# Kernel tuning notes

Measured on AMD Instinct MI355X. Metric: run time of the kernel, lower is better.

## Reference

```python
import jax, jax.numpy as jnp
import numpy as np

B, T, H = 16, 512, 384   # batch, phoneme length, hidden
F, K = 384, 3            # filter size, kernel size
DMAX = 8                 # max per-token duration
L = T * DMAX             # static max expanded length (original uses real_len.max())


def conv1d_same(x, w, b):
    # x: [B, T, Cin], w: [Cout, Cin, K] (torch OIW layout), padding = K//2 both sides
    y = jax.lax.conv_general_dilated(
        x.transpose(0, 2, 1), w, window_strides=(1,),
        padding=[(K // 2, K // 2)], dimension_numbers=('NCW', 'OIW', 'NCW'))
    return y.transpose(0, 2, 1) + b


def layer_norm(x, g, b, eps=1e-5):
    mu = jnp.mean(x, axis=-1, keepdims=True)
    var = jnp.mean(jnp.square(x - mu), axis=-1, keepdims=True)
    return (x - mu) * jax.lax.rsqrt(var + eps) * g + b


def setup_inputs() -> dict:
    key = jax.random.key(0)
    ks = jax.random.split(key, 10)
    x = jax.random.normal(ks[0], (B, T, H), dtype=jnp.float32)
    # log-durations whose exp().round() gives integers in [1, DMAX]
    dur = jax.random.randint(ks[1], (B, T), 1, DMAX + 1)
    true_durations = jnp.log(dur.astype(jnp.float32))
    s1 = 1.0 / np.sqrt(H * K)
    s2 = 1.0 / np.sqrt(F * K)
    s3 = 1.0 / np.sqrt(F)
    return {
        'x': x,
        'true_durations': true_durations,
        'conv1_w': jax.random.uniform(ks[2], (F, H, K), jnp.float32, -s1, s1),
        'conv1_b': jnp.zeros((F,), jnp.float32),
        'ln1_g': jnp.ones((F,), jnp.float32),
        'ln1_b': jnp.zeros((F,), jnp.float32),
        'conv2_w': jax.random.uniform(ks[3], (F, F, K), jnp.float32, -s2, s2),
        'conv2_b': jnp.zeros((F,), jnp.float32),
        'ln2_g': jnp.ones((F,), jnp.float32),
        'ln2_b': jnp.zeros((F,), jnp.float32),
        'lin_w': jax.random.uniform(ks[4], (F, 1), jnp.float32, -s3, s3),
        'lin_b': jnp.zeros((1,), jnp.float32),
    }


def reference(x, true_durations, conv1_w, conv1_b, ln1_g, ln1_b,
              conv2_w, conv2_b, ln2_g, ln2_b, lin_w, lin_b):
    # duration predictor net (dropout in eval mode = identity)
    h = conv1d_same(x, conv1_w, conv1_b)
    h = jax.nn.gelu(layer_norm(h, ln1_g, ln1_b), approximate=False)
    h = conv1d_same(h, conv2_w, conv2_b)
    h = jax.nn.gelu(layer_norm(h, ln2_g, ln2_b), approximate=False)
    length = jax.nn.relu(h @ lin_w + lin_b)[..., 0]  # [B, T]

    # length regulation with ground-truth durations (detached ints in original)
    dur = jnp.round(jnp.exp(true_durations)).astype(jnp.int32)  # [B, T]
    ends = jnp.cumsum(dur, axis=1)          # [B, T]
    starts = ends - dur                     # [B, T]
    k = jnp.arange(L)                       # [L]
    # binary alignment: A[b,t,l] = 1 iff starts[b,t] <= l < ends[b,t]
    A = ((k >= starts[..., None]) & (k < ends[..., None])).astype(x.dtype)  # [B,T,L]
    out = jnp.einsum('bth,btl->blh', x, A)  # = (x^T @ A)^T, [B, L, H]
    return out, length
```

## Files before the change

kernel.cpp:

```cpp
#include <hip/hip_runtime.h>
#include <stdint.h>

typedef unsigned short u16;
typedef unsigned int   u32;

#define B_    16
#define T_    512
#define H_    384
#define F_    384
#define DMAX_ 8
#define L_    4096
#define KD    1152
#define M_    8192

typedef __bf16 bf16x8 __attribute__((ext_vector_type(8)));
typedef float  f32x4  __attribute__((ext_vector_type(4)));

typedef __attribute__((address_space(1))) u32 gu32;
typedef __attribute__((address_space(3))) u32 lu32;

__device__ __forceinline__ void dma16(const void* g, void* l) {
    __builtin_amdgcn_global_load_lds((gu32*)(uintptr_t)g, (lu32*)(u32)(uintptr_t)l, 16, 0, 0);
}

__device__ __forceinline__ u16 f2b(float f) {
    union { float f; u32 i; } v; v.f = f;
    u32 x = v.i;
    return (u16)((x + 0x7fffu + ((x >> 16) & 1u)) >> 16);
}

__global__ void k_prep(const float* __restrict__ td, const float* __restrict__ w1,
                       const float* __restrict__ w2, const float* __restrict__ x,
                       int* __restrict__ tmap, u16* __restrict__ Wp1,
                       u16* __restrict__ Wp2, u16* __restrict__ xb,
                       u16* __restrict__ zp) {
    int blk = blockIdx.x, tid = threadIdx.x;
    if (blk < 16) {
        __shared__ int s[T_];
        int b = blk, t = tid;
        int d = (int)roundf(expf(td[b * T_ + t]));
        if (d < 0) d = 0; if (d > DMAX_) d = DMAX_;
        int v = d;
        s[t] = v;
        __syncthreads();
        for (int off = 1; off < T_; off <<= 1) {
            int add = (t >= off) ? s[t - off] : 0;
            __syncthreads();
            v += add;
            s[t] = v;
            __syncthreads();
        }
        int end = v, start = end - d;
        for (int i = start; i < end; ++i) tmap[b * L_ + i] = t;
        int total = s[T_ - 1];
        for (int l = total + t; l < L_; l += T_) tmap[b * L_ + l] = -1;
    } else if (blk == 16) {
        zp[tid] = 0;
    } else if (blk < 17 + 1728) {
        int j = (blk - 17) * 512 + tid;
        const int n = F_ * H_ * 3;
        const float* src = (j < n) ? w1 : w2;
        u16* dst         = (j < n) ? Wp1 : Wp2;
        int jj = (j < n) ? j : j - n;
        int f = jj / (H_ * 3);
        int rem = jj % (H_ * 3);
        int c = rem / 3, kk = rem % 3;
        dst[f * KD + kk * H_ + c] = f2b(src[jj]);
    } else {
        int v = (blk - 1745) * 512 + tid;
        float4 f = *(const float4*)(x + (size_t)v * 4);
        u16 o[4] = { f2b(f.x), f2b(f.y), f2b(f.z), f2b(f.w) };
        *(uint2*)(xb + (size_t)v * 4) = *(uint2*)o;
    }
}

__global__ void k_expand(const float* __restrict__ x, const int* __restrict__ tmap,
                         float* __restrict__ out) {
    int v = blockIdx.x * blockDim.x + threadIdx.x;
    if (v >= B_ * L_ * 96) return;
    int row = v / 96, c4 = v % 96;
    int b = row >> 12;
    int t = tmap[row];
    uint4 val = make_uint4(0u, 0u, 0u, 0u);
    if (t >= 0) val = *(const uint4*)(x + (size_t)((b << 9) + t) * H_ + c4 * 4);
    *(uint4*)(out + (size_t)row * H_ + c4 * 4) = val;
}

struct GemmCtx {
    const u16* abase[3];
    const u16* bbase[12];
    u16* destA;
    u16* destB[12];
    const u16* aptr[2][2];
    const u16* bptr[6][2];
};

__device__ __forceinline__ void gemm_core(u16* smem, const u16* __restrict__ src,
                                          const u16* __restrict__ Wp,
                                          const u16* __restrict__ zp,
                                          int m0, int tid, f32x4 acc[2][6]) {
    int w = tid >> 6, lane = tid & 63;
    int quad = lane >> 4, l16 = lane & 15;

    int rowA = tid >> 3;
    int qlA  = (tid & 7) ^ (rowA & 7);
    int arow = m0 + rowA;
    int bB = arow >> 9, tt = arow & 511;
    const u16* abase[3];
    #pragma unroll
    for (int kk = 0; kk < 3; ++kk) {
        int ts = tt + kk - 1;
        abase[kk] = (ts >= 0 && ts < T_) ? (src + (size_t)((bB << 9) + ts) * H_ + qlA * 8)
                                         : (zp + qlA * 8);
    }
    u16* destA = smem + (size_t)(w * 64) * 8;

    const u16* bbase[12];
    u16* destB[12];
    #pragma unroll
    for (int p = 0; p < 12; ++p) {
        int bc = p * 256 + tid;
        int rowB = bc >> 3;
        int qlB = (bc & 7) ^ (rowB & 7);
        bbase[p] = Wp + (size_t)rowB * KD + qlB * 8;
        destB[p] = smem + (size_t)(256 + p * 256 + w * 64) * 8;
    }

    const u16* aptr[2][2];
    #pragma unroll
    for (int i = 0; i < 2; ++i)
        #pragma unroll
        for (int kv = 0; kv < 2; ++kv) {
            int row = i * 16 + l16;
            aptr[i][kv] = smem + (size_t)((row << 3) | ((kv * 4 + quad) ^ (row & 7))) * 8;
        }
    const u16* bptr[6][2];
    #pragma unroll
    for (int j = 0; j < 6; ++j)
        #pragma unroll
        for (int kv = 0; kv < 2; ++kv) {
            int row = w * 96 + j * 16 + l16;
            bptr[j][kv] = smem + (size_t)(256 + ((row << 3) | ((kv * 4 + quad) ^ (row & 7)))) * 8;
        }

    #pragma unroll
    for (int i = 0; i < 2; ++i)
        #pragma unroll
        for (int j = 0; j < 6; ++j)
            acc[i][j] = f32x4{0.f, 0.f, 0.f, 0.f};

    for (int kk = 0; kk < 3; ++kk) {
        for (int s6 = 0; s6 < 6; ++s6) {
            int koff = kk * 384 + s6 * 64;
            dma16(abase[kk] + s6 * 64, destA);
            #pragma unroll
            for (int p = 0; p < 12; ++p) dma16(bbase[p] + koff, destB[p]);
            __syncthreads();
            #pragma unroll
            for (int kv = 0; kv < 2; ++kv) {
                bf16x8 af0 = *(const bf16x8*)aptr[0][kv];
                bf16x8 af1 = *(const bf16x8*)aptr[1][kv];
                #pragma unroll
                for (int j = 0; j < 6; ++j) {
                    bf16x8 bf = *(const bf16x8*)bptr[j][kv];
                    acc[0][j] = __builtin_amdgcn_mfma_f32_16x16x32_bf16(af0, bf, acc[0][j], 0, 0, 0);
                    acc[1][j] = __builtin_amdgcn_mfma_f32_16x16x32_bf16(af1, bf, acc[1][j], 0, 0, 0);
                }
            }
            __syncthreads();
        }
    }
}

__launch_bounds__(256)
__global__ void k_gemm1(const u16* __restrict__ xb, const u16* __restrict__ Wp,
                        const float* __restrict__ bias, const float* __restrict__ g,
                        const float* __restrict__ beta, u16* __restrict__ G,
                        const u16* __restrict__ zp) {
    __shared__ u16 smem[3328 * 8];
    int tid = threadIdx.x;
    int w = tid >> 6, lane = tid & 63;
    int quad = lane >> 4, l16 = lane & 15;
    int m0 = blockIdx.x * 32;

    f32x4 acc[2][6];
    gemm_core(smem, xb, Wp, zp, m0, tid, acc);

    float bcol[6], gcol[6], becol[6];
    #pragma unroll
    for (int j = 0; j < 6; ++j) {
        int col = w * 96 + j * 16 + l16;
        bcol[j] = bias[col]; gcol[j] = g[col]; becol[j] = beta[col];
    }
    float* sb  = (float*)smem;
    float* s2b = (float*)smem + 128;
    #pragma unroll
    for (int i = 0; i < 2; ++i)
        #pragma unroll
        for (int r = 0; r < 4; ++r) {
            float s = 0.f, s2 = 0.f;
            #pragma unroll
            for (int j = 0; j < 6; ++j) {
                float y = acc[i][j][r] + bcol[j];
                s += y; s2 += y * y;
            }
            #pragma unroll
            for (int off = 8; off; off >>= 1) { s += __shfl_down(s, off); s2 += __shfl_down(s2, off); }
            if (l16 == 0) {
                int rl = i * 16 + quad * 4 + r;
                sb[w * 32 + rl] = s; s2b[w * 32 + rl] = s2;
            }
        }
    __syncthreads();
    #pragma unroll
    for (int i = 0; i < 2; ++i)
        #pragma unroll
        for (int r = 0; r < 4; ++r) {
            int rl = i * 16 + quad * 4 + r;
            float S  = sb[rl] + sb[32 + rl] + sb[64 + rl] + sb[96 + rl];
            float S2 = s2b[rl] + s2b[32 + rl] + s2b[64 + rl] + s2b[96 + rl];
            float mean = S * (1.f / F_);
            float var  = S2 * (1.f / F_) - mean * mean;
            float rstd = rsqrtf(var + 1e-5f);
            #pragma unroll
            for (int j = 0; j < 6; ++j) {
                int col = w * 96 + j * 16 + l16;
                float y  = (acc[i][j][r] + bcol[j] - mean) * rstd * gcol[j] + becol[j];
                float gl = 0.5f * y * (1.f + erff(y * 0.70710678118654752f));
                G[(size_t)(m0 + rl) * F_ + col] = f2b(gl);
            }
        }
}

__launch_bounds__(256)
__global__ void k_gemm2(const u16* __restrict__ G, const u16* __restrict__ Wp,
                        const float* __restrict__ bias, const float* __restrict__ g,
                        const float* __restrict__ beta, const float* __restrict__ lw,
                        const float* __restrict__ lb, float* __restrict__ out1,
                        const u16* __restrict__ zp) {
    __shared__ u16 smem[3328 * 8];
    int tid = threadIdx.x;
    int w = tid >> 6, lane = tid & 63;
    int quad = lane >> 4, l16 = lane & 15;
    int m0 = blockIdx.x * 32;

    f32x4 acc[2][6];
    gemm_core(smem, G, Wp, zp, m0, tid, acc);

    float bcol[6], gcol[6], becol[6], lwcol[6];
    #pragma unroll
    for (int j = 0; j < 6; ++j) {
        int col = w * 96 + j * 16 + l16;
        bcol[j] = bias[col]; gcol[j] = g[col]; becol[j] = beta[col]; lwcol[j] = lw[col];
    }
    float* sb  = (float*)smem;
    float* s2b = (float*)smem + 128;
    float* db  = (float*)smem + 256;
    #pragma unroll
    for (int i = 0; i < 2; ++i)
        #pragma unroll
        for (int r = 0; r < 4; ++r) {
            float s = 0.f, s2 = 0.f;
            #pragma unroll
            for (int j = 0; j < 6; ++j) {
                float y = acc[i][j][r] + bcol[j];
                s += y; s2 += y * y;
            }
            #pragma unroll
            for (int off = 8; off; off >>= 1) { s += __shfl_down(s, off); s2 += __shfl_down(s2, off); }
            if (l16 == 0) {
                int rl = i * 16 + quad * 4 + r;
                sb[w * 32 + rl] = s; s2b[w * 32 + rl] = s2;
            }
        }
    __syncthreads();
    #pragma unroll
    for (int i = 0; i < 2; ++i)
        #pragma unroll
        for (int r = 0; r < 4; ++r) {
            int rl = i * 16 + quad * 4 + r;
            float S  = sb[rl] + sb[32 + rl] + sb[64 + rl] + sb[96 + rl];
            float S2 = s2b[rl] + s2b[32 + rl] + s2b[64 + rl] + s2b[96 + rl];
            float mean = S * (1.f / F_);
            float var  = S2 * (1.f / F_) - mean * mean;
            float rstd = rsqrtf(var + 1e-5f);
            float dot = 0.f;
            #pragma unroll
            for (int j = 0; j < 6; ++j) {
                float y  = (acc[i][j][r] + bcol[j] - mean) * rstd * gcol[j] + becol[j];
                float gl = 0.5f * y * (1.f + erff(y * 0.70710678118654752f));
                dot += gl * lwcol[j];
            }
            #pragma unroll
            for (int off = 8; off; off >>= 1) dot += __shfl_down(dot, off);
            if (l16 == 0) db[w * 32 + rl] = dot;
        }
    __syncthreads();
    if (tid < 32) {
        float d = db[tid] + db[32 + tid] + db[64 + tid] + db[96 + tid] + lb[0];
        out1[m0 + tid] = fmaxf(d, 0.f);
    }
}

extern "C" void kernel_launch(void* const* d_in, const int* in_sizes, int n_in,
                              void* d_out, int out_size, void* d_ws, size_t ws_size,
                              hipStream_t stream) {
    const float* x   = (const float*)d_in[0];
    const float* td  = (const float*)d_in[1];
    const float* w1  = (const float*)d_in[2];
    const float* b1  = (const float*)d_in[3];
    const float* g1  = (const float*)d_in[4];
    const float* be1 = (const float*)d_in[5];
    const float* w2  = (const float*)d_in[6];
    const float* b2  = (const float*)d_in[7];
    const float* g2  = (const float*)d_in[8];
    const float* be2 = (const float*)d_in[9];
    const float* lw  = (const float*)d_in[10];
    const float* lb  = (const float*)d_in[11];

    float* out0 = (float*)d_out;
    float* out1 = out0 + (size_t)B_ * L_ * H_;

    char* ws = (char*)d_ws;
    size_t off = 0;
    auto carve = [&](size_t bytes) -> void* {
        void* p = ws + off;
        off = (off + bytes + 255) & ~(size_t)255;
        return p;
    };
    int*  tmap = (int*)carve((size_t)B_ * L_ * sizeof(int));
    u16*  Wp1  = (u16*)carve((size_t)F_ * KD * sizeof(u16));
    u16*  Wp2  = (u16*)carve((size_t)F_ * KD * sizeof(u16));
    u16*  xb   = (u16*)carve((size_t)M_ * H_ * sizeof(u16));
    u16*  G    = (u16*)carve((size_t)M_ * F_ * sizeof(u16));
    u16*  zp   = (u16*)carve(1024);

    k_prep<<<3281, 512, 0, stream>>>(td, w1, w2, x, tmap, Wp1, Wp2, xb, zp);
    k_expand<<<(B_ * L_ * 96 + 255) / 256, 256, 0, stream>>>(x, tmap, out0);
    k_gemm1<<<M_ / 32, 256, 0, stream>>>(xb, Wp1, b1, g1, be1, G, zp);
    k_gemm2<<<M_ / 32, 256, 0, stream>>>(G, Wp2, b2, g2, be2, lw, lb, out1, zp);
}
```

Baseline: 206.1 us.

## Double-buffer LDS tiles in conv GEMMs and use eight waves per block

The GEMM core now keeps two LDS buffers and issues the async global-to-LDS loads for the next K slice before computing on the current one. This cuts the barriers to one per step and aims to hide load latency. Blocks grow from 256 to 512 threads, so each wave covers 48 output columns instead of 96, and the layernorm reductions are widened to combine 8 waves. The doubled LDS footprint may limit how many blocks fit per CU, and smaller per-wave tiles reduce register reuse.

```diff
diff --git a/kernel.cpp b/kernel.cpp
--- a/kernel.cpp
+++ b/kernel.cpp
@@ -86,121 +86,125 @@
     *(uint4*)(out + (size_t)row * H_ + c4 * 4) = val;
 }
 
-struct GemmCtx {
-    const u16* abase[3];
-    const u16* bbase[12];
-    u16* destA;
-    u16* destB[12];
-    const u16* aptr[2][2];
-    const u16* bptr[6][2];
-};
+#define CH_ 3328
 
 __device__ __forceinline__ void gemm_core(u16* smem, const u16* __restrict__ src,
                                           const u16* __restrict__ Wp,
                                           const u16* __restrict__ zp,
-                                          int m0, int tid, f32x4 acc[2][6]) {
+                                          int m0, int tid, f32x4 acc[2][3]) {
     int w = tid >> 6, lane = tid & 63;
     int quad = lane >> 4, l16 = lane & 15;
 
-    int rowA = tid >> 3;
-    int qlA  = (tid & 7) ^ (rowA & 7);
-    int arow = m0 + rowA;
-    int bB = arow >> 9, tt = arow & 511;
-    const u16* abase[3];
-    #pragma unroll
-    for (int kk = 0; kk < 3; ++kk) {
-        int ts = tt + kk - 1;
-        abase[kk] = (ts >= 0 && ts < T_) ? (src + (size_t)((bB << 9) + ts) * H_ + qlA * 8)
-                                         : (zp + qlA * 8);
-    }
-    u16* destA = smem + (size_t)(w * 64) * 8;
-
-    const u16* bbase[12];
-    u16* destB[12];
-    #pragma unroll
-    for (int p = 0; p < 12; ++p) {
-        int bc = p * 256 + tid;
+    const u16* bbase[6];
+    int bdst[6];
+    #pragma unroll
+    for (int p = 0; p < 6; ++p) {
+        int bc = p * 512 + tid;
         int rowB = bc >> 3;
         int qlB = (bc & 7) ^ (rowB & 7);
         bbase[p] = Wp + (size_t)rowB * KD + qlB * 8;
-        destB[p] = smem + (size_t)(256 + p * 256 + w * 64) * 8;
-    }
-
-    const u16* aptr[2][2];
+        bdst[p] = bc;
+    }
+    const u16* abase[3];
+    int adst = 3072 + tid;
+    {
+        int rowA = (tid & 255) >> 3;
+        int qlA = (tid & 7) ^ (rowA & 7);
+        int arow = m0 + rowA;
+        int bB = arow >> 9, tt = arow & 511;
+        #pragma unroll
+        for (int kk = 0; kk < 3; ++kk) {
+            int ts = tt + kk - 1;
+            abase[kk] = (ts >= 0 && ts < T_) ? (src + (size_t)((bB << 9) + ts) * H_ + qlA * 8)
+                                             : (zp + qlA * 8);
+        }
+    }
+
+    int aoff[2][2], boff[3][2];
     #pragma unroll
     for (int i = 0; i < 2; ++i)
         #pragma unroll
         for (int kv = 0; kv < 2; ++kv) {
             int row = i * 16 + l16;
-            aptr[i][kv] = smem + (size_t)((row << 3) | ((kv * 4 + quad) ^ (row & 7))) * 8;
-        }
-    const u16* bptr[6][2];
-    #pragma unroll
-    for (int j = 0; j < 6; ++j)
+            aoff[i][kv] = (3072 + ((row << 3) | ((kv * 4 + quad) ^ (row & 7)))) * 8;
+        }
+    #pragma unroll
+    for (int j = 0; j < 3; ++j)
         #pragma unroll
         for (int kv = 0; kv < 2; ++kv) {
-            int row = w * 96 + j * 16 + l16;
-            bptr[j][kv] = smem + (size_t)(256 + ((row << 3) | ((kv * 4 + quad) ^ (row & 7)))) * 8;
-        }
-
-    #pragma unroll
-    for (int i = 0; i < 2; ++i)
-        #pragma unroll
-        for (int j = 0; j < 6; ++j)
+            int row = w * 48 + j * 16 + l16;
+            boff[j][kv] = (((row << 3) | ((kv * 4 + quad) ^ (row & 7)))) * 8;
+        }
+
+    #pragma unroll
+    for (int i = 0; i < 2; ++i)
+        #pragma unroll
+        for (int j = 0; j < 3; ++j)
             acc[i][j] = f32x4{0.f, 0.f, 0.f, 0.f};
 
-    for (int kk = 0; kk < 3; ++kk) {
-        for (int s6 = 0; s6 < 6; ++s6) {
-            int koff = kk * 384 + s6 * 64;
-            dma16(abase[kk] + s6 * 64, destA);
-            #pragma unroll
-            for (int p = 0; p < 12; ++p) dma16(bbase[p] + koff, destB[p]);
-            __syncthreads();
-            #pragma unroll
-            for (int kv = 0; kv < 2; ++kv) {
-                bf16x8 af0 = *(const bf16x8*)aptr[0][kv];
-                bf16x8 af1 = *(const bf16x8*)aptr[1][kv];
-                #pragma unroll
-                for (int j = 0; j < 6; ++j) {
-                    bf16x8 bf = *(const bf16x8*)bptr[j][kv];
-                    acc[0][j] = __builtin_amdgcn_mfma_f32_16x16x32_bf16(af0, bf, acc[0][j], 0, 0, 0);
-                    acc[1][j] = __builtin_amdgcn_mfma_f32_16x16x32_bf16(af1, bf, acc[1][j], 0, 0, 0);
-                }
-            }
-            __syncthreads();
-        }
-    }
-}
-
-__launch_bounds__(256)
+    {
+        u16* base = smem;
+        #pragma unroll
+        for (int p = 0; p < 6; ++p) dma16(bbase[p], base + (size_t)bdst[p] * 8);
+        if (tid < 256) dma16(abase[0], base + (size_t)adst * 8);
+    }
+
+    int kk1 = 0, s61 = 0;
+    for (int s = 0; s < 18; ++s) {
+        __syncthreads();
+        if (s < 17) {
+            if (++s61 == 6) { s61 = 0; ++kk1; }
+            int koff = (s + 1) * 64;
+            u16* base = smem + (size_t)(((s + 1) & 1) ? CH_ : 0) * 8;
+            #pragma unroll
+            for (int p = 0; p < 6; ++p) dma16(bbase[p] + koff, base + (size_t)bdst[p] * 8);
+            if (tid < 256) dma16(abase[kk1] + s61 * 64, base + (size_t)adst * 8);
+        }
+        const u16* rb = smem + (size_t)((s & 1) ? CH_ : 0) * 8;
+        #pragma unroll
+        for (int kv = 0; kv < 2; ++kv) {
+            bf16x8 af0 = *(const bf16x8*)(rb + aoff[0][kv]);
+            bf16x8 af1 = *(const bf16x8*)(rb + aoff[1][kv]);
+            #pragma unroll
+            for (int j = 0; j < 3; ++j) {
+                bf16x8 bf = *(const bf16x8*)(rb + boff[j][kv]);
+                acc[0][j] = __builtin_amdgcn_mfma_f32_16x16x32_bf16(af0, bf, acc[0][j], 0, 0, 0);
+                acc[1][j] = __builtin_amdgcn_mfma_f32_16x16x32_bf16(af1, bf, acc[1][j], 0, 0, 0);
+            }
+        }
+    }
+    __syncthreads();
+}
+
+__launch_bounds__(512, 2)
 __global__ void k_gemm1(const u16* __restrict__ xb, const u16* __restrict__ Wp,
                         const float* __restrict__ bias, const float* __restrict__ g,
                         const float* __restrict__ beta, u16* __restrict__ G,
                         const u16* __restrict__ zp) {
-    __shared__ u16 smem[3328 * 8];
+    __shared__ u16 smem[2 * CH_ * 8];
     int tid = threadIdx.x;
     int w = tid >> 6, lane = tid & 63;
     int quad = lane >> 4, l16 = lane & 15;
     int m0 = blockIdx.x * 32;
 
-    f32x4 acc[2][6];
+    f32x4 acc[2][3];
     gemm_core(smem, xb, Wp, zp, m0, tid, acc);
 
-    float bcol[6], gcol[6], becol[6];
-    #pragma unroll
-    for (int j = 0; j < 6; ++j) {
-        int col = w * 96 + j * 16 + l16;
+    float bcol[3], gcol[3], becol[3];
+    #pragma unroll
+    for (int j = 0; j < 3; ++j) {
+        int col = w * 48 + j * 16 + l16;
         bcol[j] = bias[col]; gcol[j] = g[col]; becol[j] = beta[col];
     }
     float* sb  = (float*)smem;
-    float* s2b = (float*)smem + 128;
+    float* s2b = (float*)smem + 256;
     #pragma unroll
     for (int i = 0; i < 2; ++i)
         #pragma unroll
         for (int r = 0; r < 4; ++r) {
             float s = 0.f, s2 = 0.f;
             #pragma unroll
-            for (int j = 0; j < 6; ++j) {
+            for (int j = 0; j < 3; ++j) {
                 float y = acc[i][j][r] + bcol[j];
                 s += y; s2 += y * y;
             }
@@ -217,14 +221,15 @@
         #pragma unroll
         for (int r = 0; r < 4; ++r) {
             int rl = i * 16 + quad * 4 + r;
-            float S  = sb[rl] + sb[32 + rl] + sb[64 + rl] + sb[96 + rl];
-            float S2 = s2b[rl] + s2b[32 + rl] + s2b[64 + rl] + s2b[96 + rl];
+            float S = 0.f, S2 = 0.f;
+            #pragma unroll
+            for (int w2 = 0; w2 < 8; ++w2) { S += sb[w2 * 32 + rl]; S2 += s2b[w2 * 32 + rl]; }
             float mean = S * (1.f / F_);
             float var  = S2 * (1.f / F_) - mean * mean;
             float rstd = rsqrtf(var + 1e-5f);
             #pragma unroll
-            for (int j = 0; j < 6; ++j) {
-                int col = w * 96 + j * 16 + l16;
+            for (int j = 0; j < 3; ++j) {
+                int col = w * 48 + j * 16 + l16;
                 float y  = (acc[i][j][r] + bcol[j] - mean) * rstd * gcol[j] + becol[j];
                 float gl = 0.5f * y * (1.f + erff(y * 0.70710678118654752f));
                 G[(size_t)(m0 + rl) * F_ + col] = f2b(gl);
@@ -232,37 +237,37 @@
         }
 }
 
-__launch_bounds__(256)
+__launch_bounds__(512, 2)
 __global__ void k_gemm2(const u16* __restrict__ G, const u16* __restrict__ Wp,
                         const float* __restrict__ bias, const float* __restrict__ g,
                         const float* __restrict__ beta, const float* __restrict__ lw,
                         const float* __restrict__ lb, float* __restrict__ out1,
                         const u16* __restrict__ zp) {
-    __shared__ u16 smem[3328 * 8];
+    __shared__ u16 smem[2 * CH_ * 8];
     int tid = threadIdx.x;
     int w = tid >> 6, lane = tid & 63;
     int quad = lane >> 4, l16 = lane & 15;
     int m0 = blockIdx.x * 32;
 
-    f32x4 acc[2][6];
+    f32x4 acc[2][3];
     gemm_core(smem, G, Wp, zp, m0, tid, acc);
 
-    float bcol[6], gcol[6], becol[6], lwcol[6];
-    #pragma unroll
-    for (int j = 0; j < 6; ++j) {
-        int col = w * 96 + j * 16 + l16;
+    float bcol[3], gcol[3], becol[3], lwcol[3];
+    #pragma unroll
+    for (int j = 0; j < 3; ++j) {
+        int col = w * 48 + j * 16 + l16;
         bcol[j] = bias[col]; gcol[j] = g[col]; becol[j] = beta[col]; lwcol[j] = lw[col];
     }
     float* sb  = (float*)smem;
-    float* s2b = (float*)smem + 128;
-    float* db  = (float*)smem + 256;
+    float* s2b = (float*)smem + 256;
+    float* db  = (float*)smem + 512;
     #pragma unroll
     for (int i = 0; i < 2; ++i)
         #pragma unroll
         for (int r = 0; r < 4; ++r) {
             float s = 0.f, s2 = 0.f;
             #pragma unroll
-            for (int j = 0; j < 6; ++j) {
+            for (int j = 0; j < 3; ++j) {
                 float y = acc[i][j][r] + bcol[j];
                 s += y; s2 += y * y;
             }
@@ -279,14 +284,15 @@
         #pragma unroll
         for (int r = 0; r < 4; ++r) {
             int rl = i * 16 + quad * 4 + r;
-            float S  = sb[rl] + sb[32 + rl] + sb[64 + rl] + sb[96 + rl];
-            float S2 = s2b[rl] + s2b[32 + rl] + s2b[64 + rl] + s2b[96 + rl];
+            float S = 0.f, S2 = 0.f;
+            #pragma unroll
+            for (int w2 = 0; w2 < 8; ++w2) { S += sb[w2 * 32 + rl]; S2 += s2b[w2 * 32 + rl]; }
             float mean = S * (1.f / F_);
             float var  = S2 * (1.f / F_) - mean * mean;
             float rstd = rsqrtf(var + 1e-5f);
             float dot = 0.f;
             #pragma unroll
-            for (int j = 0; j < 6; ++j) {
+            for (int j = 0; j < 3; ++j) {
                 float y  = (acc[i][j][r] + bcol[j] - mean) * rstd * gcol[j] + becol[j];
                 float gl = 0.5f * y * (1.f + erff(y * 0.70710678118654752f));
                 dot += gl * lwcol[j];
@@ -297,7 +303,9 @@
         }
     __syncthreads();
     if (tid < 32) {
-        float d = db[tid] + db[32 + tid] + db[64 + tid] + db[96 + tid] + lb[0];
+        float d = lb[0];
+        #pragma unroll
+        for (int w2 = 0; w2 < 8; ++w2) d += db[w2 * 32 + tid];
         out1[m0 + tid] = fmaxf(d, 0.f);
     }
 }
@@ -337,6 +345,6 @@
 
     k_prep<<<3281, 512, 0, stream>>>(td, w1, w2, x, tmap, Wp1, Wp2, xb, zp);
     k_expand<<<(B_ * L_ * 96 + 255) / 256, 256, 0, stream>>>(x, tmap, out0);
-    k_gemm1<<<M_ / 32, 256, 0, stream>>>(xb, Wp1, b1, g1, be1, G, zp);
-    k_gemm2<<<M_ / 32, 256, 0, stream>>>(G, Wp2, b2, g2, be2, lw, lb, out1, zp);
-}
+    k_gemm1<<<M_ / 32, 512, 0, stream>>>(xb, Wp1, b1, g1, be1, G, zp);
+    k_gemm2<<<M_ / 32, 512, 0, stream>>>(G, Wp2, b2, g2, be2, lw, lb, out1, zp);
+}
```

Measured after the change: 187.3 us. -9.1%, faster.
